# Kernel tuning notes

Measured on AMD Instinct MI355X. Metric: run time of the kernel, lower is better.

Reference implementation:

```python
import jax, jax.numpy as jnp
import numpy as np

EPS = 1e-12  # torch F.normalize default eps


def setup_inputs() -> dict:
    key = jax.random.key(0)
    k1, k2, k3 = jax.random.split(key, 3)
    ns, d_in, n_feat, n_classes = 16384, 512, 256, 1000
    x = jax.random.normal(k1, (ns, d_in), dtype=jnp.float32)
    W = jax.random.normal(k2, (d_in, n_feat), dtype=jnp.float32) * 0.05
    # class prototypes: L2-normalized embeddings, one per seen class (seen_c == n_classes)
    means = jax.random.normal(k3, (n_classes, n_feat), dtype=jnp.float32)
    means = means / jnp.maximum(jnp.linalg.norm(means, axis=1, keepdims=True), EPS)
    return {"x": x, "W": W, "means": means, "t": 0}


def reference(x, W, means, t):
    # forward_training: backbone + L2 normalization along feature dim
    feats = x @ W                                   # [ns, n_feat]
    preds = feats / jnp.maximum(jnp.linalg.norm(feats, axis=1, keepdims=True), EPS)
    # deployment forward: nearest prototype by negative dot product
    # original: per-sample dist = -means @ pred^T; dist.min(0) -> class index
    dist = -(preds @ means.T)                       # [ns, seen_c]
    classpred = jnp.argmin(dist, axis=1)            # first min on ties, matches torch
    n_classes = means.shape[0]
    out = jax.nn.one_hot(classpred, n_classes, dtype=jnp.float32)  # [ns, n_classes]
    return out
```

## Files before the change

kernel.cpp:

```cpp
#include <hip/hip_runtime.h>
#include <float.h>

#define NS   16384
#define K1   512
#define F    256
#define NC   1000
#define SPB  32
#define NTHR 512
#define NBLK (NS / SPB)


typedef _Float16 half8  __attribute__((ext_vector_type(8)));
typedef float    float4v __attribute__((ext_vector_type(4)));
typedef float    float2v __attribute__((ext_vector_type(2)));

#define M_OFF 262144

__global__ void prep(const float* __restrict__ W, const float* __restrict__ means,
                     _Float16* __restrict__ ws) {
    int g = blockIdx.x * blockDim.x + threadIdx.x;
    if (g < 16384) {
        int lane = g & 63, tile = g >> 6;
        int ks = tile >> 4, nt = tile & 15;
        int k0 = ks * 32 + (lane >> 4) * 8;
        int n  = nt * 16 + (lane & 15);
        half8 hv, lv;
#pragma unroll
        for (int j = 0; j < 8; ++j) {
            float v = W[(size_t)(k0 + j) * F + n] * 16.0f;
            _Float16 hi = (_Float16)v;
            hv[j] = hi;
            lv[j] = (_Float16)(v - (float)hi);
        }
        _Float16* d = ws + (size_t)tile * 1024 + (size_t)lane * 8;
        *reinterpret_cast<half8*>(d)       = hv;
        *reinterpret_cast<half8*>(d + 512) = lv;
    } else {
        int gm = g - 16384;
        int lane = gm & 63, tile = gm >> 6;
        int ks = tile >> 6, gt = tile & 63;
        int k0 = ks * 32 + (lane >> 4) * 8;
        int c  = gt * 16 + (lane & 15);
        half8 hv, lv;
#pragma unroll
        for (int j = 0; j < 8; ++j) {
            float v = (c < NC) ? means[(size_t)c * F + k0 + j] * 16.0f : 0.0f;
            _Float16 hi = (_Float16)v;
            hv[j] = hi;
            lv[j] = (_Float16)(v - (float)hi);
        }
        _Float16* d = ws + M_OFF + (size_t)tile * 1024 + (size_t)lane * 8;
        *reinterpret_cast<half8*>(d)       = hv;
        *reinterpret_cast<half8*>(d + 512) = lv;
    }
}

#define MFMA(a, b, c) __builtin_amdgcn_mfma_f32_16x16x32_f16((a), (b), (c), 0, 0, 0)

__attribute__((amdgpu_flat_work_group_size(NTHR, NTHR), amdgpu_waves_per_eu(2, 4)))
__global__ void fused_mfma(const float* __restrict__ x,
                           const _Float16* __restrict__ ws,
                           float* __restrict__ out) {
    __shared__ _Float16 xsh[2][32][44];
    __shared__ _Float16 xsl[2][32][44];
    __shared__ _Float16 fh[32][264];
    __shared__ _Float16 fl[32][264];
    __shared__ float cand_v[32][8];
    __shared__ int   cand_i[32][8];
    __shared__ int   bidx[32];

    const int tid  = threadIdx.x;
    const int lane = tid & 63;
    const int w    = tid >> 6;
    const int quad = lane >> 4;
    const int cl   = lane & 15;
    const int s0   = blockIdx.x * SPB;

    const int xrow = tid >> 4;
    const int xc   = (tid & 15) * 2;

    float4v acc1[2][2];
#pragma unroll
    for (int p = 0; p < 2; ++p)
#pragma unroll
        for (int mt = 0; mt < 2; ++mt)
            acc1[p][mt] = (float4v){0.f, 0.f, 0.f, 0.f};

    const _Float16* wsrc = ws + ((size_t)(w * 2) << 10) + ((size_t)lane << 3);
    half8 wbh[2][2], wbl[2][2];
#pragma unroll
    for (int p = 0; p < 2; ++p) {
        wbh[0][p] = *reinterpret_cast<const half8*>(wsrc + p * 1024);
        wbl[0][p] = *reinterpret_cast<const half8*>(wsrc + p * 1024 + 512);
    }

    float2v xv = __builtin_nontemporal_load(
        reinterpret_cast<const float2v*>(x + (size_t)(s0 + xrow) * K1 + xc));

#pragma unroll
    for (int ks = 0; ks < 16; ++ks) {
        const int buf = ks & 1;
        {
            float vx = xv.x * 8.0f, vy = xv.y * 8.0f;
            _Float16 hx = (_Float16)vx, hy = (_Float16)vy;
            xsh[buf][xrow][xc]     = hx;
            xsh[buf][xrow][xc + 1] = hy;
            xsl[buf][xrow][xc]     = (_Float16)(vx - (float)hx);
            xsl[buf][xrow][xc + 1] = (_Float16)(vy - (float)hy);
        }
        if (ks < 15)
            xv = __builtin_nontemporal_load(
                reinterpret_cast<const float2v*>(
                    x + (size_t)(s0 + xrow) * K1 + (ks + 1) * 32 + xc));
        __syncthreads();
        if (ks < 15) {
#pragma unroll
            for (int p = 0; p < 2; ++p) {
                wbh[buf ^ 1][p] = *reinterpret_cast<const half8*>(
                    wsrc + (size_t)(ks + 1) * 16384 + p * 1024);
                wbl[buf ^ 1][p] = *reinterpret_cast<const half8*>(
                    wsrc + (size_t)(ks + 1) * 16384 + p * 1024 + 512);
            }
        }
        half8 ah[2], al[2];
#pragma unroll
        for (int mt = 0; mt < 2; ++mt) {
            ah[mt] = *reinterpret_cast<const half8*>(&xsh[buf][mt * 16 + cl][quad * 8]);
            al[mt] = *reinterpret_cast<const half8*>(&xsl[buf][mt * 16 + cl][quad * 8]);
        }
#pragma unroll
        for (int p = 0; p < 2; ++p)
#pragma unroll
            for (int mt = 0; mt < 2; ++mt) {
                acc1[p][mt] = MFMA(ah[mt], wbh[buf][p], acc1[p][mt]);
                acc1[p][mt] = MFMA(ah[mt], wbl[buf][p], acc1[p][mt]);
                acc1[p][mt] = MFMA(al[mt], wbh[buf][p], acc1[p][mt]);
            }
    }

#pragma unroll
    for (int p = 0; p < 2; ++p)
#pragma unroll
        for (int mt = 0; mt < 2; ++mt)
#pragma unroll
            for (int r = 0; r < 4; ++r) {
                int srow = mt * 16 + quad * 4 + r;
                int n    = (w * 2 + p) * 16 + cl;
                float v  = acc1[p][mt][r];
                _Float16 hi = (_Float16)v;
                fh[srow][n] = hi;
                fl[srow][n] = (_Float16)(v - (float)hi);
            }
    __syncthreads();

    float4v acc2[2][8];
#pragma unroll
    for (int mt = 0; mt < 2; ++mt)
#pragma unroll
        for (int nt = 0; nt < 8; ++nt)
            acc2[mt][nt] = (float4v){0.f, 0.f, 0.f, 0.f};

    const _Float16* mbase = ws + M_OFF + ((size_t)(w * 8) << 10) + ((size_t)lane << 3);

    half8 mh[2][2], ml[2][2];
    half8 fah[2][2], fal[2][2];
#pragma unroll
    for (int t = 0; t < 2; ++t) {
        mh[0][t] = *reinterpret_cast<const half8*>(mbase + t * 1024);
        ml[0][t] = *reinterpret_cast<const half8*>(mbase + t * 1024 + 512);
    }
#pragma unroll
    for (int mt = 0; mt < 2; ++mt) {
        fah[0][mt] = *reinterpret_cast<const half8*>(&fh[mt * 16 + cl][quad * 8]);
        fal[0][mt] = *reinterpret_cast<const half8*>(&fl[mt * 16 + cl][quad * 8]);
    }

#pragma unroll
    for (int b = 0; b < 32; ++b) {
        const int cb = b & 1;
        const int ks = b >> 2;
        const int ab = ks & 1;
        if (b < 31) {
            const int b2 = b + 1;
            const _Float16* src =
                mbase + (size_t)((b2 >> 2) * 65536 + (b2 & 3) * 2048);
#pragma unroll
            for (int t = 0; t < 2; ++t) {
                mh[cb ^ 1][t] = *reinterpret_cast<const half8*>(src + t * 1024);
                ml[cb ^ 1][t] = *reinterpret_cast<const half8*>(src + t * 1024 + 512);
            }
        }
        if ((b & 3) == 2 && ks < 7) {
#pragma unroll
            for (int mt = 0; mt < 2; ++mt) {
                fah[ab ^ 1][mt] = *reinterpret_cast<const half8*>(
                    &fh[mt * 16 + cl][(ks + 1) * 32 + quad * 8]);
                fal[ab ^ 1][mt] = *reinterpret_cast<const half8*>(
                    &fl[mt * 16 + cl][(ks + 1) * 32 + quad * 8]);
            }
        }
        const int n0 = (b & 3) * 2;
#pragma unroll
        for (int t = 0; t < 2; ++t) {
            const int nt = n0 + t;
#pragma unroll
            for (int mt = 0; mt < 2; ++mt) {
                acc2[mt][nt] = MFMA(fah[ab][mt], mh[cb][t], acc2[mt][nt]);
                acc2[mt][nt] = MFMA(fah[ab][mt], ml[cb][t], acc2[mt][nt]);
                acc2[mt][nt] = MFMA(fal[ab][mt], mh[cb][t], acc2[mt][nt]);
            }
        }
    }

#pragma unroll
    for (int mt = 0; mt < 2; ++mt)
#pragma unroll
        for (int r = 0; r < 4; ++r) {
            float v  = -FLT_MAX;
            int   ix = 0x7FFFFFFF;
#pragma unroll
            for (int nt = 0; nt < 8; ++nt) {
                int c = (w * 8 + nt) * 16 + cl;
                if (c < NC) {
                    float sc = acc2[mt][nt][r];
                    if (sc > v) { v = sc; ix = c; }
                }
            }
#pragma unroll
            for (int off = 1; off < 16; off <<= 1) {
                float ov = __shfl_xor(v, off, 64);
                int   oi = __shfl_xor(ix, off, 64);
                if (ov > v || (ov == v && oi < ix)) { v = ov; ix = oi; }
            }
            if (cl == 0) {
                int srow = mt * 16 + quad * 4 + r;
                cand_v[srow][w] = v;
                cand_i[srow][w] = ix;
            }
        }
    __syncthreads();

    if (tid < 32) {
        float v  = cand_v[tid][0];
        int   ix = cand_i[tid][0];
#pragma unroll
        for (int q = 1; q < 8; ++q) {
            float ov = cand_v[tid][q];
            int   oi = cand_i[tid][q];
            if (ov > v || (ov == v && oi < ix)) { v = ov; ix = oi; }
        }
        bidx[tid] = ix;
    }
    __syncthreads();

    const int NF4 = NC / 4;
    for (int q = tid; q < SPB * NF4; q += NTHR) {
        int row   = q / NF4;
        int c4    = q - row * NF4;
        int b     = bidx[row];
        int cbase = c4 * 4;
        float4v v;
        v.x = (cbase + 0 == b) ? 1.f : 0.f;
        v.y = (cbase + 1 == b) ? 1.f : 0.f;
        v.z = (cbase + 2 == b) ? 1.f : 0.f;
        v.w = (cbase + 3 == b) ? 1.f : 0.f;
        __builtin_nontemporal_store(
            v, reinterpret_cast<float4v*>(out + (size_t)(s0 + row) * NC + cbase));
    }
}

extern "C" void kernel_launch(void* const* d_in, const int* in_sizes, int n_in,
                              void* d_out, int out_size, void* d_ws, size_t ws_size,
                              hipStream_t stream) {
    const float* x     = (const float*)d_in[0];
    const float* W     = (const float*)d_in[1];
    const float* means = (const float*)d_in[2];
    float* out         = (float*)d_out;
    _Float16* ws       = (_Float16*)d_ws;

    prep<<<192, 256, 0, stream>>>(W, means, ws);
    fused_mfma<<<NBLK, NTHR, 0, stream>>>(x, ws, out);
}
```

Baseline: 140.2 us.

## Double rows per block and overlap zero-fill output stores with second GEMM

Raises samples per block from 32 to 64, so each loaded W/means fragment feeds twice as many MFMAs and the weight traffic per sample is halved. The x load is widened to float4 per thread. The one-hot output is now written as zeros interleaved into the second GEMM's k-loop, followed by a single scattered store of 1.0 per row, so the output stores overlap MFMA work instead of running as a tail phase. This relies on the write ordering of the zero stores and the later 1.0 store within the block, and the larger accumulator arrays raise register pressure and may lower occupancy.

```diff
diff --git a/kernel.cpp b/kernel.cpp
--- a/kernel.cpp
+++ b/kernel.cpp
@@ -5,14 +5,13 @@
 #define K1   512
 #define F    256
 #define NC   1000
-#define SPB  32
+#define SPB  64
 #define NTHR 512
 #define NBLK (NS / SPB)
 
 
 typedef _Float16 half8  __attribute__((ext_vector_type(8)));
 typedef float    float4v __attribute__((ext_vector_type(4)));
-typedef float    float2v __attribute__((ext_vector_type(2)));
 
 #define M_OFF 262144
 
@@ -61,13 +60,13 @@
 __global__ void fused_mfma(const float* __restrict__ x,
                            const _Float16* __restrict__ ws,
                            float* __restrict__ out) {
-    __shared__ _Float16 xsh[2][32][44];
-    __shared__ _Float16 xsl[2][32][44];
-    __shared__ _Float16 fh[32][264];
-    __shared__ _Float16 fl[32][264];
-    __shared__ float cand_v[32][8];
-    __shared__ int   cand_i[32][8];
-    __shared__ int   bidx[32];
+    __shared__ _Float16 xsh[2][64][40];
+    __shared__ _Float16 xsl[2][64][40];
+    __shared__ _Float16 fh[64][264];
+    __shared__ _Float16 fl[64][264];
+    __shared__ float cand_v[64][8];
+    __shared__ int   cand_i[64][8];
+    __shared__ int   bidx[64];
 
     const int tid  = threadIdx.x;
     const int lane = tid & 63;
@@ -76,14 +75,14 @@
     const int cl   = lane & 15;
     const int s0   = blockIdx.x * SPB;
 
-    const int xrow = tid >> 4;
-    const int xc   = (tid & 15) * 2;
-
-    float4v acc1[2][2];
+    const int xrow = tid >> 3;
+    const int xc4  = (tid & 7) * 4;
+
+    float4v acc1[2][4];
 #pragma unroll
     for (int p = 0; p < 2; ++p)
 #pragma unroll
-        for (int mt = 0; mt < 2; ++mt)
+        for (int mt = 0; mt < 4; ++mt)
             acc1[p][mt] = (float4v){0.f, 0.f, 0.f, 0.f};
 
     const _Float16* wsrc = ws + ((size_t)(w * 2) << 10) + ((size_t)lane << 3);
@@ -94,24 +93,25 @@
         wbl[0][p] = *reinterpret_cast<const half8*>(wsrc + p * 1024 + 512);
     }
 
-    float2v xv = __builtin_nontemporal_load(
-        reinterpret_cast<const float2v*>(x + (size_t)(s0 + xrow) * K1 + xc));
+    float4v xv = __builtin_nontemporal_load(
+        reinterpret_cast<const float4v*>(x + (size_t)(s0 + xrow) * K1 + xc4));
 
 #pragma unroll
     for (int ks = 0; ks < 16; ++ks) {
         const int buf = ks & 1;
         {
-            float vx = xv.x * 8.0f, vy = xv.y * 8.0f;
-            _Float16 hx = (_Float16)vx, hy = (_Float16)vy;
-            xsh[buf][xrow][xc]     = hx;
-            xsh[buf][xrow][xc + 1] = hy;
-            xsl[buf][xrow][xc]     = (_Float16)(vx - (float)hx);
-            xsl[buf][xrow][xc + 1] = (_Float16)(vy - (float)hy);
+#pragma unroll
+            for (int j = 0; j < 4; ++j) {
+                float v = xv[j] * 8.0f;
+                _Float16 hi = (_Float16)v;
+                xsh[buf][xrow][xc4 + j] = hi;
+                xsl[buf][xrow][xc4 + j] = (_Float16)(v - (float)hi);
+            }
         }
         if (ks < 15)
             xv = __builtin_nontemporal_load(
-                reinterpret_cast<const float2v*>(
-                    x + (size_t)(s0 + xrow) * K1 + (ks + 1) * 32 + xc));
+                reinterpret_cast<const float4v*>(
+                    x + (size_t)(s0 + xrow) * K1 + (ks + 1) * 32 + xc4));
         __syncthreads();
         if (ks < 15) {
 #pragma unroll
@@ -122,16 +122,16 @@
                     wsrc + (size_t)(ks + 1) * 16384 + p * 1024 + 512);
             }
         }
-        half8 ah[2], al[2];
-#pragma unroll
-        for (int mt = 0; mt < 2; ++mt) {
+        half8 ah[4], al[4];
+#pragma unroll
+        for (int mt = 0; mt < 4; ++mt) {
             ah[mt] = *reinterpret_cast<const half8*>(&xsh[buf][mt * 16 + cl][quad * 8]);
             al[mt] = *reinterpret_cast<const half8*>(&xsl[buf][mt * 16 + cl][quad * 8]);
         }
 #pragma unroll
         for (int p = 0; p < 2; ++p)
 #pragma unroll
-            for (int mt = 0; mt < 2; ++mt) {
+            for (int mt = 0; mt < 4; ++mt) {
                 acc1[p][mt] = MFMA(ah[mt], wbh[buf][p], acc1[p][mt]);
                 acc1[p][mt] = MFMA(ah[mt], wbl[buf][p], acc1[p][mt]);
                 acc1[p][mt] = MFMA(al[mt], wbh[buf][p], acc1[p][mt]);
@@ -141,7 +141,7 @@
 #pragma unroll
     for (int p = 0; p < 2; ++p)
 #pragma unroll
-        for (int mt = 0; mt < 2; ++mt)
+        for (int mt = 0; mt < 4; ++mt)
 #pragma unroll
             for (int r = 0; r < 4; ++r) {
                 int srow = mt * 16 + quad * 4 + r;
@@ -153,67 +153,64 @@
             }
     __syncthreads();
 
-    float4v acc2[2][8];
-#pragma unroll
-    for (int mt = 0; mt < 2; ++mt)
-#pragma unroll
-        for (int nt = 0; nt < 8; ++nt)
-            acc2[mt][nt] = (float4v){0.f, 0.f, 0.f, 0.f};
+    float4v acc2[4][8];
+#pragma unroll
+    for (int mt = 0; mt < 4; ++mt)
+#pragma unroll
+        for (int gt = 0; gt < 8; ++gt)
+            acc2[mt][gt] = (float4v){0.f, 0.f, 0.f, 0.f};
 
     const _Float16* mbase = ws + M_OFF + ((size_t)(w * 8) << 10) + ((size_t)lane << 3);
 
-    half8 mh[2][2], ml[2][2];
-    half8 fah[2][2], fal[2][2];
-#pragma unroll
-    for (int t = 0; t < 2; ++t) {
-        mh[0][t] = *reinterpret_cast<const half8*>(mbase + t * 1024);
-        ml[0][t] = *reinterpret_cast<const half8*>(mbase + t * 1024 + 512);
-    }
-#pragma unroll
-    for (int mt = 0; mt < 2; ++mt) {
-        fah[0][mt] = *reinterpret_cast<const half8*>(&fh[mt * 16 + cl][quad * 8]);
-        fal[0][mt] = *reinterpret_cast<const half8*>(&fl[mt * 16 + cl][quad * 8]);
-    }
-
-#pragma unroll
-    for (int b = 0; b < 32; ++b) {
-        const int cb = b & 1;
-        const int ks = b >> 2;
-        const int ab = ks & 1;
-        if (b < 31) {
-            const int b2 = b + 1;
-            const _Float16* src =
-                mbase + (size_t)((b2 >> 2) * 65536 + (b2 & 3) * 2048);
-#pragma unroll
-            for (int t = 0; t < 2; ++t) {
-                mh[cb ^ 1][t] = *reinterpret_cast<const half8*>(src + t * 1024);
-                ml[cb ^ 1][t] = *reinterpret_cast<const half8*>(src + t * 1024 + 512);
-            }
-        }
-        if ((b & 3) == 2 && ks < 7) {
-#pragma unroll
-            for (int mt = 0; mt < 2; ++mt) {
-                fah[ab ^ 1][mt] = *reinterpret_cast<const half8*>(
-                    &fh[mt * 16 + cl][(ks + 1) * 32 + quad * 8]);
-                fal[ab ^ 1][mt] = *reinterpret_cast<const half8*>(
-                    &fl[mt * 16 + cl][(ks + 1) * 32 + quad * 8]);
-            }
-        }
-        const int n0 = (b & 3) * 2;
-#pragma unroll
-        for (int t = 0; t < 2; ++t) {
-            const int nt = n0 + t;
-#pragma unroll
-            for (int mt = 0; mt < 2; ++mt) {
-                acc2[mt][nt] = MFMA(fah[ab][mt], mh[cb][t], acc2[mt][nt]);
-                acc2[mt][nt] = MFMA(fah[ab][mt], ml[cb][t], acc2[mt][nt]);
-                acc2[mt][nt] = MFMA(fal[ab][mt], mh[cb][t], acc2[mt][nt]);
-            }
-        }
-    }
-
-#pragma unroll
-    for (int mt = 0; mt < 2; ++mt)
+    half8 mh[2], ml[2];
+    mh[0] = *reinterpret_cast<const half8*>(mbase);
+    ml[0] = *reinterpret_cast<const half8*>(mbase + 512);
+
+    const float4v z4 = (float4v){0.f, 0.f, 0.f, 0.f};
+    const int NF4 = NC / 4;
+
+#pragma unroll
+    for (int ks = 0; ks < 8; ++ks) {
+        half8 fah[4], fal[4];
+#pragma unroll
+        for (int mt = 0; mt < 4; ++mt) {
+            fah[mt] = *reinterpret_cast<const half8*>(
+                &fh[mt * 16 + cl][ks * 32 + quad * 8]);
+            fal[mt] = *reinterpret_cast<const half8*>(
+                &fl[mt * 16 + cl][ks * 32 + quad * 8]);
+        }
+#pragma unroll
+        for (int j = 0; j < 4; ++j) {
+            int q = (ks * 4 + j) * NTHR + tid;
+            if (q < SPB * NF4) {
+                int row = q / NF4;
+                int c4  = q - row * NF4;
+                __builtin_nontemporal_store(
+                    z4, reinterpret_cast<float4v*>(
+                            out + (size_t)(s0 + row) * NC + c4 * 4));
+            }
+        }
+#pragma unroll
+        for (int gt = 0; gt < 8; ++gt) {
+            const int ii = ks * 8 + gt;
+            const int cb = ii & 1;
+            if (ii < 63) {
+                const _Float16* src = mbase +
+                    (size_t)(((ii + 1) >> 3) * 65536 + ((ii + 1) & 7) * 1024);
+                mh[cb ^ 1] = *reinterpret_cast<const half8*>(src);
+                ml[cb ^ 1] = *reinterpret_cast<const half8*>(src + 512);
+            }
+#pragma unroll
+            for (int mt = 0; mt < 4; ++mt) {
+                acc2[mt][gt] = MFMA(fah[mt], mh[cb], acc2[mt][gt]);
+                acc2[mt][gt] = MFMA(fah[mt], ml[cb], acc2[mt][gt]);
+                acc2[mt][gt] = MFMA(fal[mt], mh[cb], acc2[mt][gt]);
+            }
+        }
+    }
+
+#pragma unroll
+    for (int mt = 0; mt < 4; ++mt)
 #pragma unroll
         for (int r = 0; r < 4; ++r) {
             float v  = -FLT_MAX;
@@ -240,7 +237,7 @@
         }
     __syncthreads();
 
-    if (tid < 32) {
+    if (tid < SPB) {
         float v  = cand_v[tid][0];
         int   ix = cand_i[tid][0];
 #pragma unroll
@@ -253,20 +250,8 @@
     }
     __syncthreads();
 
-    const int NF4 = NC / 4;
-    for (int q = tid; q < SPB * NF4; q += NTHR) {
-        int row   = q / NF4;
-        int c4    = q - row * NF4;
-        int b     = bidx[row];
-        int cbase = c4 * 4;
-        float4v v;
-        v.x = (cbase + 0 == b) ? 1.f : 0.f;
-        v.y = (cbase + 1 == b) ? 1.f : 0.f;
-        v.z = (cbase + 2 == b) ? 1.f : 0.f;
-        v.w = (cbase + 3 == b) ? 1.f : 0.f;
-        __builtin_nontemporal_store(
-            v, reinterpret_cast<float4v*>(out + (size_t)(s0 + row) * NC + cbase));
-    }
+    if (tid < SPB)
+        out[(size_t)(s0 + tid) * NC + bidx[tid]] = 1.0f;
 }
 
 extern "C" void kernel_launch(void* const* d_in, const int* in_sizes, int n_in,
```

Result: faster. 132.1 us (-5.8%).
